# Optimization experiments

Hardware: AMD Instinct MI355X
Metric: run time of the kernel (lower is better)

The kernel has to match this reference:

```python
import jax, jax.numpy as jnp
import numpy as np

D = 1024
H = 16
B = 8
N = 1024


def setup_inputs() -> dict:
    key = jax.random.key(0)
    k1, k2, k3 = jax.random.split(key, 3)
    x = jax.random.normal(k1, (B, N, D), dtype=jnp.float32)
    w_in = jax.random.normal(k2, (D, 3 * D), dtype=jnp.float32) * (1.0 / np.sqrt(D))
    w_out = jax.random.normal(k3, (D, D), dtype=jnp.float32) * (1.0 / np.sqrt(D))
    b_out = jnp.zeros((D,), dtype=jnp.float32)
    return {"x": x, "w_in": w_in, "w_out": w_out, "b_out": b_out}


def reference(x, w_in, w_out, b_out):
    h = H
    d = D // H
    scale = D ** (-0.5)  # note: full dimension, per source
    qkv = x @ w_in  # [B, N, 3D]
    # rearrange 'b n (qkv h d) -> qkv b h n d'
    qkv = qkv.reshape(x.shape[0], x.shape[1], 3, h, d)
    qkv = jnp.transpose(qkv, (2, 0, 3, 1, 4))
    q, k, v = qkv[0], qkv[1], qkv[2]
    scores = jnp.einsum('bhid,bhjd->bhij', q, k) * scale
    attn = jax.nn.softmax(scores, axis=-1)
    out = jnp.einsum('bhij,bhjd->bhid', attn, v)
    # 'b h n d -> b n (h d)'
    out = jnp.transpose(out, (0, 2, 1, 3)).reshape(x.shape[0], x.shape[1], h * d)
    return out @ w_out + b_out
```

## Files before the change

kernel.cpp:

```cpp
#include <hip/hip_runtime.h>
#include <stdint.h>
#include <stddef.h>

typedef __bf16 bf16;
typedef __bf16 bf16x4 __attribute__((ext_vector_type(4)));
typedef __bf16 bf16x8 __attribute__((ext_vector_type(8)));
typedef float  f32x4  __attribute__((ext_vector_type(4)));
typedef float  f32x16 __attribute__((ext_vector_type(16)));
typedef float  f32x4v __attribute__((ext_vector_type(4)));

__device__ __forceinline__ void gload_lds16(const void* g, void* lds) {
  __builtin_amdgcn_global_load_lds(
      (__attribute__((address_space(1))) void*)(uintptr_t)g,
      (__attribute__((address_space(3))) void*)lds,
      16, 0, 0);
}


__global__ __launch_bounds__(256) void prep_inputs(
    const float* __restrict__ x,     bf16* __restrict__ xb,
    const float* __restrict__ w_in,  bf16* __restrict__ wint,
    const float* __restrict__ w_out, bf16* __restrict__ woutt)
{
  __shared__ bf16 tile[32][33];
  const int bid = blockIdx.x, tid = threadIdx.x;

  if (bid < 8192) {
    int i = bid * 1024 + tid * 4;
    f32x4v v = *reinterpret_cast<const f32x4v*>(x + i);
    bf16x4 o;
    o[0] = (bf16)v[0]; o[1] = (bf16)v[1]; o[2] = (bf16)v[2]; o[3] = (bf16)v[3];
    *reinterpret_cast<bf16x4*>(xb + i) = o;
    return;
  }

  const float* in; bf16* out; int R, C, c0, r0;
  if (bid < 11264) {
    int t = bid - 8192;
    in = w_in; out = wint; R = 1024; C = 3072;
    c0 = (t % 96) * 32; r0 = (t / 96) * 32;
  } else {
    int t = bid - 11264;
    in = w_out; out = woutt; R = 1024; C = 1024;
    c0 = (t % 32) * 32; r0 = (t / 32) * 32;
  }
  const int tx = tid & 31, ty = tid >> 5;
  #pragma unroll
  for (int i = ty; i < 32; i += 8)
    tile[i][tx] = (bf16)in[(size_t)(r0 + i) * C + (c0 + tx)];
  __syncthreads();
  #pragma unroll
  for (int i = ty; i < 32; i += 8)
    out[(size_t)(c0 + i) * R + (r0 + tx)] = tile[tx][i];
}


template <typename OT, bool BIAS>
__global__ __launch_bounds__(256) void gemm_abt(
    const bf16* __restrict__ A,
    const bf16* __restrict__ Bt,
    const float* __restrict__ bias,
    OT* __restrict__ C, int M, int N, int K)
{
  __shared__ bf16 As[128 * 64];
  __shared__ bf16 Bs[128 * 64];

  const int tid = threadIdx.x;
  const int w = tid >> 6, l = tid & 63;
  const int l15 = l & 15, l4 = l >> 4, l7 = l & 7;
  const int wr = w >> 1, wc = w & 1;

  const int nwgx = N >> 7;
  const int nwg  = (M >> 7) * nwgx;
  const int cpx  = nwg >> 3;
  const int bid  = blockIdx.x;
  const int swz  = (bid & 7) * cpx + (bid >> 3);
  const int m0 = (swz / nwgx) * 128, n0 = (swz % nwgx) * 128;

  f32x4 acc[4][4];
  #pragma unroll
  for (int i = 0; i < 4; i++)
    #pragma unroll
    for (int j = 0; j < 4; j++) acc[i][j] = (f32x4){0.f, 0.f, 0.f, 0.f};

  const int srow  = w * 8 + (l >> 3);
  const int sslot = (l & 7) ^ ((l >> 3) & 7);
  const int KT = K >> 6;

  for (int kt = 0; kt < KT; ++kt) {
    __syncthreads();
    const int kcol = kt * 64 + sslot * 8;
    #pragma unroll
    for (int p = 0; p < 4; ++p) {
      gload_lds16(A  + (size_t)(m0 + p * 32 + srow) * K + kcol,
                  (char*)As + p * 4096 + w * 1024);
      gload_lds16(Bt + (size_t)(n0 + p * 32 + srow) * K + kcol,
                  (char*)Bs + p * 4096 + w * 1024);
    }
    __syncthreads();

    #pragma unroll
    for (int kk = 0; kk < 2; ++kk) {
      const int coff = (kk * 32 + l4 * 8) ^ (l7 << 3);
      bf16x8 af[4], bq[4];
      #pragma unroll
      for (int m = 0; m < 4; ++m) {
        int r = wr * 64 + m * 16 + l15;
        af[m] = *reinterpret_cast<const bf16x8*>(&As[r * 64 + coff]);
      }
      #pragma unroll
      for (int n = 0; n < 4; ++n) {
        int r = wc * 64 + n * 16 + l15;
        bq[n] = *reinterpret_cast<const bf16x8*>(&Bs[r * 64 + coff]);
      }
      #pragma unroll
      for (int m = 0; m < 4; ++m)
        #pragma unroll
        for (int n = 0; n < 4; ++n)
          acc[m][n] = __builtin_amdgcn_mfma_f32_16x16x32_bf16(af[m], bq[n], acc[m][n], 0, 0, 0);
    }
  }

  #pragma unroll
  for (int m = 0; m < 4; ++m) {
    #pragma unroll
    for (int n = 0; n < 4; ++n) {
      int col = n0 + wc * 64 + n * 16 + l15;
      float bv = BIAS ? bias[col] : 0.f;
      #pragma unroll
      for (int j = 0; j < 4; ++j) {
        int row = m0 + wr * 64 + m * 16 + l4 * 4 + j;
        float v = acc[m][n][j] + bv;
        if constexpr (BIAS)
          __builtin_nontemporal_store((OT)v, &C[(size_t)row * N + col]);
        else
          C[(size_t)row * N + col] = (OT)v;
      }
    }
  }
}


__global__ __launch_bounds__(512) void attn_fused(
    const bf16* __restrict__ qkv,
    bf16* __restrict__ aout)
{
  __shared__ bf16 Ks[64 * 64];
  __shared__ bf16 Vt[64 * 64];
  __shared__ bf16 Pl[8][32 * 64];

  const int tid = threadIdx.x;
  const int w = tid >> 6, l = tid & 63;
  const int l31 = l & 31, hi = l >> 5;

  const int bid = blockIdx.x;
  const int c  = bid & 7, rr = bid >> 3;
  const int g  = c * 16 + (rr & 15);
  const int qt = rr >> 4;
  const int h  = g & 15;
  const int b  = g >> 4;

  const bf16* base = qkv + (size_t)b * 1024 * 3072;
  const int qrow0 = qt * 256 + w * 32;

  const float qscale = 0.03125f * 1.44269504f;
  bf16x8 qf[4];
  #pragma unroll
  for (int st = 0; st < 4; st++) {
    const bf16* p = base + (size_t)(qrow0 + l31) * 3072 + h * 64 + st * 16 + hi * 8;
    bf16x8 v = *reinterpret_cast<const bf16x8*>(p);
    #pragma unroll
    for (int e = 0; e < 8; e++) v[e] = (bf16)((float)v[e] * qscale);
    qf[st] = v;
  }

  bf16x8 onesf;
  #pragma unroll
  for (int e = 0; e < 8; e++) onesf[e] = (bf16)1.0f;

  f32x16 acc0 = {}, acc1 = {}, accS = {};

  const int skey  = w * 8 + (l >> 3);
  const int sslot = (l & 7) ^ ((l >> 3) & 7);
  const int vd0   = (tid & 15) * 4;
  const int vk0   = ((tid >> 4) & 15) * 4;
  const int vslot = (tid >> 5) & 7;
  const int vhalf = (tid >> 4) & 1;

  for (int kt = 0; kt < 16; ++kt) {
    __syncthreads();
    gload_lds16(base + (size_t)(kt * 64 + skey) * 3072 + 1024 + h * 64 + sslot * 8,
                (char*)Ks + w * 1024);
    if (tid < 256) {
      bf16x4 vv[4];
      #pragma unroll
      for (int i = 0; i < 4; ++i)
        vv[i] = *reinterpret_cast<const bf16x4*>(
            base + (size_t)(kt * 64 + vk0 + i) * 3072 + 2048 + h * 64 + vd0);
      #pragma unroll
      for (int j = 0; j < 4; ++j) {
        int d = vd0 + j;
        bf16x4 o; o[0] = vv[0][j]; o[1] = vv[1][j]; o[2] = vv[2][j]; o[3] = vv[3][j];
        *reinterpret_cast<bf16x4*>(
            &Vt[d * 64 + ((vslot ^ (d & 7) ^ ((d >> 3) & 7)) * 8 + vhalf * 4)]) = o;
      }
    }
    __syncthreads();

    #pragma unroll
    for (int ktile = 0; ktile < 2; ++ktile) {
      f32x16 s = {};
      const int key = ktile * 32 + l31;
      #pragma unroll
      for (int st = 0; st < 4; ++st) {
        const int slot = (2 * st + hi) ^ (key & 7);
        bf16x8 kf = *reinterpret_cast<const bf16x8*>(&Ks[key * 64 + slot * 8]);
        s = __builtin_amdgcn_mfma_f32_32x32x16_bf16(kf, qf[st], s, 0, 0, 0);
      }
      #pragma unroll
      for (int gq = 0; gq < 4; ++gq) {
        bf16x4 pb;
        #pragma unroll
        for (int j2 = 0; j2 < 4; ++j2) {
          float pv = __builtin_amdgcn_exp2f(s[4 * gq + j2]);
          pb[j2] = (bf16)pv;
        }
        const int chunk = ktile * 4 + gq;
        *reinterpret_cast<bf16x4*>(
            &Pl[w][l31 * 64 + ((chunk ^ (l31 & 7)) * 8 + hi * 4)]) = pb;
      }
    }

    const int d7x0 = (l31 & 7) ^ (l31 >> 3);
    const int d7x1 = d7x0 ^ 4;
    #pragma unroll
    for (int st = 0; st < 4; ++st) {
      const int cs = 2 * st + hi;
      bf16x8 pa  = *reinterpret_cast<const bf16x8*>(
          &Pl[w][l31 * 64 + ((cs ^ (l31 & 7)) * 8)]);
      accS = __builtin_amdgcn_mfma_f32_32x32x16_bf16(pa, onesf, accS, 0, 0, 0);
      bf16x8 vf0 = *reinterpret_cast<const bf16x8*>(
          &Vt[l31 * 64 + ((cs ^ d7x0) * 8)]);
      acc0 = __builtin_amdgcn_mfma_f32_32x32x16_bf16(pa, vf0, acc0, 0, 0, 0);
      bf16x8 vf1 = *reinterpret_cast<const bf16x8*>(
          &Vt[(32 + l31) * 64 + ((cs ^ d7x1) * 8)]);
      acc1 = __builtin_amdgcn_mfma_f32_32x32x16_bf16(pa, vf1, acc1, 0, 0, 0);
    }
  }

  #pragma unroll
  for (int reg = 0; reg < 16; ++reg) {
    int q_r = (reg & 3) + 8 * (reg >> 2) + 4 * hi;
    float rinv = 1.0f / accS[reg];
    size_t rowoff = ((size_t)b * 1024 + qrow0 + q_r) * 1024 + h * 64;
    aout[rowoff + l31]      = (bf16)(acc0[reg] * rinv);
    aout[rowoff + 32 + l31] = (bf16)(acc1[reg] * rinv);
  }
}


extern "C" void kernel_launch(void* const* d_in, const int* in_sizes, int n_in,
                              void* d_out, int out_size, void* d_ws, size_t ws_size,
                              hipStream_t stream) {
  const float* x     = (const float*)d_in[0];
  const float* w_in  = (const float*)d_in[1];
  const float* w_out = (const float*)d_in[2];
  const float* b_out = (const float*)d_in[3];
  float* out = (float*)d_out;

  bf16* xb    = (bf16*)d_ws;
  bf16* wint  = xb    + (size_t)8192 * 1024;
  bf16* woutt = wint  + (size_t)3072 * 1024;
  bf16* qkv   = woutt + (size_t)1024 * 1024;
  bf16* ao    = qkv   + (size_t)8192 * 3072;

  prep_inputs<<<12288, 256, 0, stream>>>(x, xb, w_in, wint, w_out, woutt);

  gemm_abt<bf16, false><<<1536, 256, 0, stream>>>(xb, wint, nullptr, qkv, 8192, 3072, 1024);

  attn_fused<<<512, 512, 0, stream>>>(qkv, ao);

  gemm_abt<float, true><<<512, 256, 0, stream>>>(ao, woutt, b_out, out, 8192, 1024, 1024);
}
```

Baseline: 156.5 us.

## Use 256x256 double-buffered ping-pong GEMM kernel for QKV projection

Adds a new GEMM kernel with 256x256 tiles, 512 threads and double-buffered LDS. It interleaves asynchronous global-to-LDS loads with MFMA phases separated by barriers, and raises wave priority during the math phases. It replaces the 128x128 kernel for the QKV projection only. The aim is better data reuse per tile and overlap of memory traffic with compute. In exchange the launch drops to 384 workgroups (about 1.5 waves on 256 CUs) and runs at occupancy 1.

```diff
diff --git a/kernel.cpp b/kernel.cpp
--- a/kernel.cpp
+++ b/kernel.cpp
@@ -57,10 +57,8 @@
 
 template <typename OT, bool BIAS>
 __global__ __launch_bounds__(256) void gemm_abt(
-    const bf16* __restrict__ A,
-    const bf16* __restrict__ Bt,
-    const float* __restrict__ bias,
-    OT* __restrict__ C, int M, int N, int K)
+    const bf16* __restrict__ A, const bf16* __restrict__ Bt,
+    const float* __restrict__ bias, OT* __restrict__ C, int M, int N, int K)
 {
   __shared__ bf16 As[128 * 64];
   __shared__ bf16 Bs[128 * 64];
@@ -138,6 +136,140 @@
       }
     }
   }
+}
+
+
+template <typename OT, bool BIAS>
+__global__ __launch_bounds__(512, 1) void gemm256p(
+    const bf16* __restrict__ A,
+    const bf16* __restrict__ Bt,
+    const float* __restrict__ bias,
+    OT* __restrict__ C, int M, int N, int K)
+{
+  __shared__ bf16 As[2][256 * 64];
+  __shared__ bf16 Bs[2][256 * 64];
+
+  const int tid = threadIdx.x;
+  const int w = tid >> 6, l = tid & 63;
+  const int l15 = l & 15, l4 = l >> 4, l7 = l & 7;
+  const int wm = w >> 2, wn = w & 3;
+
+  const int nwgx = N >> 8;
+  const int nwg  = (M >> 8) * nwgx;
+  const int cpx  = nwg >> 3;
+  const int bid  = blockIdx.x;
+  const int swz  = (bid & 7) * cpx + (bid >> 3);
+  const int m0 = (swz / nwgx) * 256, n0 = (swz % nwgx) * 256;
+
+  f32x4 acc[8][4];
+  #pragma unroll
+  for (int i = 0; i < 8; i++)
+    #pragma unroll
+    for (int j = 0; j < 4; j++) acc[i][j] = (f32x4){0.f, 0.f, 0.f, 0.f};
+
+  const int w8l   = w * 8 + (l >> 3);
+  const int sslot = (l & 7) ^ ((l >> 3) & 7);
+
+  #define SA(t, q) gload_lds16(A  + (size_t)(m0 + (q) * 64 + w8l) * K + (t) * 64 + sslot * 8, \
+                               (char*)As[(t) & 1] + (q) * 8192 + w * 1024)
+  #define SB(t, u) gload_lds16(Bt + (size_t)(n0 + (u) * 64 + w8l) * K + (t) * 64 + sslot * 8, \
+                               (char*)Bs[(t) & 1] + (u) * 8192 + w * 1024)
+  #define BAR()  asm volatile("s_barrier" ::: "memory")
+  #define VM(n)  asm volatile("s_waitcnt vmcnt(" #n ")" ::: "memory")
+
+  bf16x8 afr[4][2], bfr[2][2][2];
+
+  #define LDA(buf, mh)                                                          \
+    _Pragma("unroll")                                                           \
+    for (int i = 0; i < 4; ++i)                                                 \
+      _Pragma("unroll")                                                         \
+      for (int kk = 0; kk < 2; ++kk)                                            \
+        afr[i][kk] = *reinterpret_cast<const bf16x8*>(                          \
+            &As[buf][(wm * 128 + (mh) * 64 + i * 16 + l15) * 64 +               \
+                     (((kk * 4 + l4) ^ l7) * 8)]);
+  #define LDB(buf, nh)                                                          \
+    _Pragma("unroll")                                                           \
+    for (int n2 = 0; n2 < 2; ++n2)                                              \
+      _Pragma("unroll")                                                         \
+      for (int kk = 0; kk < 2; ++kk)                                            \
+        bfr[nh][n2][kk] = *reinterpret_cast<const bf16x8*>(                     \
+            &Bs[buf][(wn * 64 + (nh) * 32 + n2 * 16 + l15) * 64 +               \
+                     (((kk * 4 + l4) ^ l7) * 8)]);
+  #define MM(mh, nh)                                                            \
+    __builtin_amdgcn_s_setprio(1);                                              \
+    _Pragma("unroll")                                                           \
+    for (int i = 0; i < 4; ++i)                                                 \
+      _Pragma("unroll")                                                         \
+      for (int n2 = 0; n2 < 2; ++n2)                                            \
+        _Pragma("unroll")                                                       \
+        for (int kk = 0; kk < 2; ++kk)                                          \
+          acc[(mh) * 4 + i][(nh) * 2 + n2] =                                    \
+              __builtin_amdgcn_mfma_f32_16x16x32_bf16(                          \
+                  afr[i][kk], bfr[nh][n2][kk],                                  \
+                  acc[(mh) * 4 + i][(nh) * 2 + n2], 0, 0, 0);                   \
+    __builtin_amdgcn_s_setprio(0);
+
+  SA(0, 0); SA(0, 2); SA(0, 1); SA(0, 3);
+  SB(0, 0); SB(0, 1); SB(0, 2); SB(0, 3);
+  SA(1, 0); SA(1, 2);
+  SB(1, 0); SB(1, 1); SB(1, 2); SB(1, 3);
+  VM(6);
+  BAR();
+
+  for (int it = 0; it < 8; ++it) {
+    const int t0 = 2 * it, t1 = 2 * it + 1;
+    const bool more = (it < 7);
+    LDA(0, 0); LDB(0, 0);
+    SA(t1, 1); SA(t1, 3);
+    BAR(); MM(0, 0) BAR();
+    LDB(0, 1);
+    if (more) { SA(t0 + 2, 0); SA(t0 + 2, 2); }
+    VM(10);
+    BAR(); MM(0, 1) BAR();
+    LDA(0, 1);
+    if (more) { SB(t0 + 2, 0); SB(t0 + 2, 1); }
+    BAR(); MM(1, 0) BAR();
+    if (more) { SB(t0 + 2, 2); SB(t0 + 2, 3); }
+    VM(8);
+    BAR(); MM(1, 1) BAR();
+    LDA(1, 0); LDB(1, 0);
+    if (more) { SA(t0 + 2, 1); SA(t0 + 2, 3); }
+    BAR(); MM(0, 0) BAR();
+    LDB(1, 1);
+    if (more) { SA(t1 + 2, 0); SA(t1 + 2, 2); }
+    VM(10);
+    BAR(); MM(0, 1) BAR();
+    LDA(1, 1);
+    if (more) { SB(t1 + 2, 0); SB(t1 + 2, 1); }
+    BAR(); MM(1, 0) BAR();
+    if (more) { SB(t1 + 2, 2); SB(t1 + 2, 3); }
+    VM(8);
+    BAR(); MM(1, 1) BAR();
+  }
+  #undef SA
+  #undef SB
+  #undef BAR
+  #undef VM
+  #undef LDA
+  #undef LDB
+  #undef MM
+
+  #pragma unroll
+  for (int mh = 0; mh < 2; ++mh)
+    #pragma unroll
+    for (int i = 0; i < 4; ++i)
+      #pragma unroll
+      for (int nh = 0; nh < 2; ++nh)
+        #pragma unroll
+        for (int n2 = 0; n2 < 2; ++n2) {
+          int col = n0 + wn * 64 + nh * 32 + n2 * 16 + l15;
+          float bv = BIAS ? bias[col] : 0.f;
+          #pragma unroll
+          for (int j = 0; j < 4; ++j) {
+            int row = m0 + wm * 128 + mh * 64 + i * 16 + l4 * 4 + j;
+            C[(size_t)row * N + col] = (OT)(acc[mh * 4 + i][nh * 2 + n2][j] + bv);
+          }
+        }
 }
 
 
@@ -276,7 +408,7 @@
 
   prep_inputs<<<12288, 256, 0, stream>>>(x, xb, w_in, wint, w_out, woutt);
 
-  gemm_abt<bf16, false><<<1536, 256, 0, stream>>>(xb, wint, nullptr, qkv, 8192, 3072, 1024);
+  gemm256p<bf16, false><<<384, 512, 0, stream>>>(xb, wint, nullptr, qkv, 8192, 3072, 1024);
 
   attn_fused<<<512, 512, 0, stream>>>(qkv, ao);
 
```

New measurement: 157.4 us. About the same (+0.6%).
